# Kernel optimization log

Hardware: AMD Instinct MI355X
Metric: run time of the kernel (lower is better)

The kernel has to match this reference:

```python
import jax, jax.numpy as jnp
import numpy as np

# Model dims (match init_kwargs)
B, L, D = 1, 2048, 1024
DI = 2048          # D_inner
N = 16             # SSM state size
DR = 64            # delta_rank
K = 4              # conv_1d_size
EPS = 1e-5
DELTA_MIN, DELTA_MAX, DELTA_FLOOR = 1e-3, 1e-1, 1e-4


def setup_inputs() -> dict:
    key = jax.random.key(0)
    ks = jax.random.split(key, 9)
    g = lambda i, shape, scale: (jax.random.normal(ks[i], shape, jnp.float32) * scale)
    x = g(0, (B, L, D), 1.0)
    rms_w = jnp.ones((D,), jnp.float32)
    in_proj_w = g(1, (D, 2 * DI), D ** -0.5)           # Linear D -> 2*DI, no bias
    conv_w = g(2, (DI, K), 0.3)                         # depthwise conv kernel
    conv_b = g(3, (DI,), 0.1)
    bcd_w = g(4, (DI, 2 * N + DR), DI ** -0.5)          # to_BCdelta, no bias
    dup_w = g(5, (DR, DI), DR ** -0.5)                  # delta_upscale weight
    # delta_upscale bias: inverse-softplus of log-uniform samples in [delta_min, delta_max]
    u = jax.random.uniform(ks[6], (DI,), jnp.float32)
    samples = jnp.clip(jnp.exp(u * (np.log(DELTA_MAX) - np.log(DELTA_MIN)) + np.log(DELTA_MIN)), DELTA_FLOOR)
    dup_b = samples + jnp.log(-jnp.expm1(-samples))
    # log(-A) with A = -[1..N] repeated over channels (S4D-real init)
    log_minus_A = jnp.tile(jnp.log(jnp.arange(1, N + 1, dtype=jnp.float32))[None, :], (DI, 1))
    D_param = jnp.ones((DI,), jnp.float32)              # skip parameter D
    out_proj_w = g(7, (DI, D), DI ** -0.5)              # Linear DI -> D, no bias
    return {"x": x, "rms_w": rms_w, "in_proj_w": in_proj_w, "conv_w": conv_w,
            "conv_b": conv_b, "bcd_w": bcd_w, "dup_w": dup_w, "dup_b": dup_b,
            "log_minus_A": log_minus_A, "D_param": D_param, "out_proj_w": out_proj_w}


def reference(x, rms_w, in_proj_w, conv_w, conv_b, bcd_w, dup_w, dup_b,
              log_minus_A, D_param, out_proj_w):
    b, l, _ = x.shape
    # RMSNorm
    xn = x * jax.lax.rsqrt(jnp.mean(x * x, axis=-1, keepdims=True) + EPS) * rms_w
    # in_proj and split into ssm branch / gating residual branch
    proj = xn @ in_proj_w                                  # (b,l,2*DI)
    xs, res = proj[..., :DI], proj[..., DI:]
    # causal depthwise conv1d (torch pads K-1 both sides then truncates -> left-pad only)
    xp = jnp.pad(xs, ((0, 0), (K - 1, 0), (0, 0)))         # (b,l+K-1,DI)
    conv = sum(xp[:, k:k + l, :] * conv_w[:, k] for k in range(K)) + conv_b
    xc = jax.nn.silu(conv)                                 # (b,l,DI)
    # S6 block
    bcd = xc @ bcd_w                                       # (b,l,DR+2N)
    delta_lr = bcd[..., :DR]
    Bm = bcd[..., DR:DR + N]                               # (b,l,N)
    Cm = bcd[..., DR + N:]                                 # (b,l,N)
    delta = jax.nn.softplus(delta_lr @ dup_w + dup_b)      # (b,l,DI)
    A = -jnp.exp(log_minus_A)                              # (DI,N)
    A_bar = jnp.exp(jnp.einsum('bld,dn->bldn', delta, A))  # (b,l,DI,N)
    B_bar_x = jnp.einsum('bld,bln,bld->bldn', delta, Bm, xc)
    # sequential selective scan: h_t = A_bar_t * h_{t-1} + B_bar_x_t
    def step(h, ab_bx):
        ab, bx = ab_bx
        h = ab * h + bx
        return h, h
    h0 = jnp.zeros((b, DI, N), x.dtype)
    _, hs = jax.lax.scan(step, h0, (jnp.swapaxes(A_bar, 0, 1), jnp.swapaxes(B_bar_x, 0, 1)))
    # hs: (l,b,DI,N); project out with C and add skip D
    y = jnp.einsum('bln,lbdn->bld', Cm, hs) + xc * D_param
    # gate, out_proj, residual
    y = y * jax.nn.silu(res)
    return y @ out_proj_w + x
```

## Files before the change

### kernel.cpp

```cpp
#include <hip/hip_runtime.h>
#include <hip/hip_bf16.h>
#include <math.h>

#define Lseq 2048
#define Dmod 1024
#define DI   2048
#define Nst  16
#define DRr  64
#define NCHUNK 32
#define LCHUNK 64
#define SPLITK 16
#define OSPLIT 4

typedef unsigned short u16;
typedef float  f32x4  __attribute__((ext_vector_type(4)));
typedef short  short8 __attribute__((ext_vector_type(8)));

__device__ __forceinline__ float sigmoidf_(float x) { return 1.f / (1.f + expf(-x)); }
__device__ __forceinline__ float softplusf_(float x) {
    return fmaxf(x, 0.f) + log1pf(expf(-fabsf(x)));
}
__device__ __forceinline__ u16 f2bf(float x) {
    union { float f; unsigned u; } v; v.f = x;
    unsigned r = (v.u + 0x7fffu + ((v.u >> 16) & 1u)) >> 16;
    return (u16)r;
}
__device__ __forceinline__ float bf2f(u16 h) {
    union { unsigned u; float f; } v; v.u = ((unsigned)h) << 16; return v.f;
}
__device__ __forceinline__ void async16(const void* g, void* l) {
    __builtin_amdgcn_global_load_lds((__attribute__((address_space(1))) void*)g,
                                     (__attribute__((address_space(3))) void*)l, 16, 0, 0);
}

struct __align__(8) u16x4 { u16 x, y, z, w; };

__global__ __launch_bounds__(256) void rmsnorm_split_k(const float* __restrict__ x,
                                                       const float* __restrict__ w,
                                                       u16* __restrict__ xh,
                                                       u16* __restrict__ xl) {
    int row = blockIdx.x;
    int tid = threadIdx.x;
    float4 v = reinterpret_cast<const float4*>(x + (size_t)row * Dmod)[tid];
    float ss = v.x * v.x + v.y * v.y + v.z * v.z + v.w * v.w;
    #pragma unroll
    for (int m = 32; m >= 1; m >>= 1) ss += __shfl_xor(ss, m);
    __shared__ float s4[4];
    if ((tid & 63) == 0) s4[tid >> 6] = ss;
    __syncthreads();
    float tot = s4[0] + s4[1] + s4[2] + s4[3];
    float scale = rsqrtf(tot * (1.0f / Dmod) + 1e-5f);
    float4 wv = reinterpret_cast<const float4*>(w)[tid];
    float o[4] = {v.x * scale * wv.x, v.y * scale * wv.y,
                  v.z * scale * wv.z, v.w * scale * wv.w};
    u16x4 H, L;
    u16* hp = &H.x; u16* lp = &L.x;
    #pragma unroll
    for (int q = 0; q < 4; q++) {
        u16 h = f2bf(o[q]); hp[q] = h; lp[q] = f2bf(o[q] - bf2f(h));
    }
    reinterpret_cast<u16x4*>(xh + (size_t)row * Dmod)[tid] = H;
    reinterpret_cast<u16x4*>(xl + (size_t)row * Dmod)[tid] = L;
}

__device__ __forceinline__ void wsplit_body(const float* __restrict__ W, int R, int Cn,
                                            int bx, int by, float (*t)[33],
                                            u16* __restrict__ Th, u16* __restrict__ Tl) {
    int r0 = by * 32, c0 = bx * 32;
    int tr = threadIdx.x >> 3;
    int tc4 = (threadIdx.x & 7) * 4;
    float4 v = *reinterpret_cast<const float4*>(&W[(size_t)(r0 + tr) * Cn + c0 + tc4]);
    t[tr][tc4 + 0] = v.x; t[tr][tc4 + 1] = v.y;
    t[tr][tc4 + 2] = v.z; t[tr][tc4 + 3] = v.w;
    __syncthreads();
    u16x4 H, L;
    u16* hp = &H.x; u16* lp = &L.x;
    #pragma unroll
    for (int q = 0; q < 4; q++) {
        float xv = t[tc4 + q][tr];
        u16 h = f2bf(xv); hp[q] = h; lp[q] = f2bf(xv - bf2f(h));
    }
    size_t o = (size_t)(c0 + tr) * R + r0 + tc4;
    *reinterpret_cast<u16x4*>(&Th[o]) = H;
    *reinterpret_cast<u16x4*>(&Tl[o]) = L;
}

__global__ __launch_bounds__(256) void wsplitT_k(const float* __restrict__ W, int R, int Cn,
                                                 u16* __restrict__ Th, u16* __restrict__ Tl) {
    __shared__ float t[32][33];
    wsplit_body(W, R, Cn, blockIdx.x, blockIdx.y, t, Th, Tl);
}

__global__ __launch_bounds__(256) void wsplit3_k(const float* __restrict__ Wo,
                                                 const float* __restrict__ Wb,
                                                 const float* __restrict__ Wd,
                                                 u16* WoH, u16* WoL,
                                                 u16* bwTH, u16* bwTL,
                                                 u16* dwTH, u16* dwTL) {
    __shared__ float t[32][33];
    int b = blockIdx.x;
    if (b < 2048) {
        wsplit_body(Wo, 2048, 1024, b & 31, b >> 5, t, WoH, WoL);
    } else if (b < 2240) {
        int bb = b - 2048;
        wsplit_body(Wb, 2048, 96, bb % 3, bb / 3, t, bwTH, bwTL);
    } else {
        int bb = b - 2240;
        wsplit_body(Wd, 64, 2048, bb & 63, bb >> 6, t, dwTH, dwTL);
    }
}

template <int BM, int BN, int EPI>
__global__ __launch_bounds__(256) void gemm_mfma3(
    const u16* __restrict__ Ah, const u16* __restrict__ Al,
    const u16* __restrict__ Bh, const u16* __restrict__ Bl,
    float* __restrict__ C, float* __restrict__ C2, const float* __restrict__ aux,
    int M, int N, int K) {
    constexpr int BK = 32;
    constexpr int MF = BM / 32, NF = BN / 32;
    constexpr int CH_A = BM / 16, CH_B = BN / 16;
    __shared__ u16 AhT[BM][BK], AlT[BM][BK], BhT[BN][BK], BlT[BN][BK];
    const int tid = threadIdx.x, lane = tid & 63, wid = tid >> 6;
    const int wr = wid >> 1, wc = wid & 1;
    const int lr = lane & 15, lk = (lane >> 4) * 8;
    const int bm0 = blockIdx.y * BM, bn0 = blockIdx.x * BN;
    const int srow = lane >> 2, scol = (lane & 3) * 8;

    int kbeg = 0, kend = K;
    if (EPI == 5) {
        int ks = K / gridDim.z;
        kbeg = blockIdx.z * ks;
        kend = kbeg + ks;
    }

    f32x4 acc[MF][NF];
    #pragma unroll
    for (int i = 0; i < MF; i++)
        #pragma unroll
        for (int j = 0; j < NF; j++) acc[i][j] = (f32x4){0.f, 0.f, 0.f, 0.f};

    for (int k0 = kbeg; k0 < kend; k0 += BK) {
        int ci = 0;
        #pragma unroll
        for (int c = 0; c < CH_A; c++, ci++) if ((ci & 3) == wid) {
            size_t g = (size_t)(bm0 + c * 16 + srow) * K + (k0 + scol);
            async16(Ah + g, (u16*)&AhT[0][0] + c * 512 + lane * 8);
        }
        #pragma unroll
        for (int c = 0; c < CH_A; c++, ci++) if ((ci & 3) == wid) {
            size_t g = (size_t)(bm0 + c * 16 + srow) * K + (k0 + scol);
            async16(Al + g, (u16*)&AlT[0][0] + c * 512 + lane * 8);
        }
        #pragma unroll
        for (int c = 0; c < CH_B; c++, ci++) if ((ci & 3) == wid) {
            size_t g = (size_t)(bn0 + c * 16 + srow) * K + (k0 + scol);
            async16(Bh + g, (u16*)&BhT[0][0] + c * 512 + lane * 8);
        }
        #pragma unroll
        for (int c = 0; c < CH_B; c++, ci++) if ((ci & 3) == wid) {
            size_t g = (size_t)(bn0 + c * 16 + srow) * K + (k0 + scol);
            async16(Bl + g, (u16*)&BlT[0][0] + c * 512 + lane * 8);
        }
        __syncthreads();

        short8 ah[MF], al[MF], bh[NF], bl[NF];
        #pragma unroll
        for (int i = 0; i < MF; i++) {
            int r = wr * (MF * 16) + i * 16 + lr;
            ah[i] = *(const short8*)&AhT[r][lk];
            al[i] = *(const short8*)&AlT[r][lk];
        }
        #pragma unroll
        for (int j = 0; j < NF; j++) {
            int r = wc * (NF * 16) + j * 16 + lr;
            bh[j] = *(const short8*)&BhT[r][lk];
            bl[j] = *(const short8*)&BlT[r][lk];
        }
        #pragma unroll
        for (int i = 0; i < MF; i++)
            #pragma unroll
            for (int j = 0; j < NF; j++) {
                acc[i][j] = __builtin_amdgcn_mfma_f32_16x16x32_bf16(ah[i], bh[j], acc[i][j], 0, 0, 0);
                acc[i][j] = __builtin_amdgcn_mfma_f32_16x16x32_bf16(ah[i], bl[j], acc[i][j], 0, 0, 0);
                acc[i][j] = __builtin_amdgcn_mfma_f32_16x16x32_bf16(al[i], bh[j], acc[i][j], 0, 0, 0);
            }
        __syncthreads();
    }

    float* Cp = C;
    if (EPI == 5) Cp = C + (size_t)blockIdx.z * M * N;
    #pragma unroll
    for (int i = 0; i < MF; i++)
        #pragma unroll
        for (int j = 0; j < NF; j++) {
            int rowg = bm0 + wr * (MF * 16) + i * 16 + (lane >> 4) * 4;
            int colg = bn0 + wc * (NF * 16) + j * 16 + lr;
            #pragma unroll
            for (int q = 0; q < 4; q++) {
                float v = acc[i][j][q];
                if (EPI == 5) {
                    Cp[(size_t)(rowg + q) * N + colg] = v;
                } else if (EPI == 2) {
                    C[(size_t)(rowg + q) * N + colg] = softplusf_(v + aux[colg]);
                } else if (EPI == 4) {
                    if (colg < DI) C[(size_t)(rowg + q) * DI + colg] = v;
                    else C2[(size_t)(rowg + q) * DI + (colg - DI)] = v * sigmoidf_(v);
                }
            }
        }
}

__global__ __launch_bounds__(256) void bcd_reduce_k(const float* __restrict__ partial,
                                                    float* __restrict__ bcd,
                                                    u16* __restrict__ bH,
                                                    u16* __restrict__ bL) {
    const int NT = Lseq * 96;
    int t = blockIdx.x * 256 + threadIdx.x;
    float s = 0.f;
    #pragma unroll
    for (int z = 0; z < SPLITK; z++) s += partial[(size_t)z * NT + t];
    bcd[t] = s;
    int col = t % 96, row = t / 96;
    if (col < DRr) {
        u16 h = f2bf(s);
        bH[(size_t)row * DRr + col] = h;
        bL[(size_t)row * DRr + col] = f2bf(s - bf2f(h));
    }
}

__global__ __launch_bounds__(256) void out_reduce_k(const float* __restrict__ part,
                                                    const float* __restrict__ x,
                                                    float* __restrict__ out) {
    int t = blockIdx.x * 256 + threadIdx.x;
    const size_t NT = (size_t)Lseq * Dmod;
    float4 xv = reinterpret_cast<const float4*>(x)[t];
    float4 o = xv;
    #pragma unroll
    for (int z = 0; z < OSPLIT; z++) {
        float4 p = reinterpret_cast<const float4*>(part + (size_t)z * NT)[t];
        o.x += p.x; o.y += p.y; o.z += p.z; o.w += p.w;
    }
    reinterpret_cast<float4*>(out)[t] = o;
}

__global__ __launch_bounds__(256) void conv_silu_k(const float* __restrict__ xs,
                                                   const float* __restrict__ cw,
                                                   const float* __restrict__ cb,
                                                   u16* __restrict__ xcH,
                                                   u16* __restrict__ xcL) {
    int d = blockIdx.x * 256 + threadIdx.x;
    int l = blockIdx.y;
    float4 w = reinterpret_cast<const float4*>(cw)[d];
    float wk[4] = {w.x, w.y, w.z, w.w};
    float s = cb[d];
    #pragma unroll
    for (int k = 0; k < 4; k++) {
        int ls = l - 3 + k;
        if (ls >= 0) s = fmaf(xs[(size_t)ls * DI + d], wk[k], s);
    }
    float v = s * sigmoidf_(s);
    size_t o = (size_t)l * DI + d;
    u16 h = f2bf(v);
    xcH[o] = h;
    xcL[o] = f2bf(v - bf2f(h));
}

__global__ __launch_bounds__(256) void scan1_k(const float* __restrict__ delta,
                                               const u16* __restrict__ xcH,
                                               const u16* __restrict__ xcL,
                                               const float* __restrict__ bcd,
                                               const float* __restrict__ lmA,
                                               float* __restrict__ Pb,
                                               float* __restrict__ Sb) {
    __shared__ float Bs[LCHUNK][16];
    const int tid = threadIdx.x;
    const int d = (blockIdx.x * 256 + tid) >> 1;
    const int half = tid & 1;
    const int c = blockIdx.y;
    const int l0 = c * LCHUNK;
    {
        int row = tid >> 2, q = (tid & 3) * 4;
        float4 v = *reinterpret_cast<const float4*>(&bcd[(size_t)(l0 + row) * 96 + DRr + q]);
        *reinterpret_cast<float4*>(&Bs[row][q]) = v;
    }
    __syncthreads();
    float negA[8], h[8];
    #pragma unroll
    for (int j = 0; j < 8; j++) {
        negA[j] = -__expf(lmA[(size_t)d * Nst + half * 8 + j]);
        h[j] = 0.f;
    }
    float sdv = 0.f;
    for (int l = 0; l < LCHUNK; ++l) {
        size_t o = (size_t)(l0 + l) * DI + d;
        float dv = delta[o];
        float xcv = bf2f(xcH[o]) + bf2f(xcL[o]);
        sdv += dv;
        float dvx = dv * xcv;
        #pragma unroll
        for (int j = 0; j < 8; j++) {
            float a = __expf(dv * negA[j]);
            h[j] = fmaf(a, h[j], dvx * Bs[l][half * 8 + j]);
        }
    }
    size_t base = ((size_t)c * DI + d) * Nst + half * 8;
    #pragma unroll
    for (int j = 0; j < 8; j++) {
        Pb[base + j] = __expf(sdv * negA[j]);
        Sb[base + j] = h[j];
    }
}

__global__ __launch_bounds__(256) void scan2_k(float* __restrict__ PH,
                                               const float* __restrict__ Sb) {
    int t = blockIdx.x * 256 + threadIdx.x;
    float H = 0.f;
    for (int c = 0; c < NCHUNK; c++) {
        size_t idx = (size_t)c * (DI * Nst) + t;
        float P = PH[idx], S = Sb[idx];
        PH[idx] = H;
        H = S + P * H;
    }
}

__global__ __launch_bounds__(256) void scan3_k(const float* __restrict__ delta,
                                               const u16* __restrict__ xcH,
                                               const u16* __restrict__ xcL,
                                               const float* __restrict__ bcd,
                                               const float* __restrict__ lmA,
                                               const float* __restrict__ Dp,
                                               const float* __restrict__ gate,
                                               const float* __restrict__ Hinit,
                                               u16* __restrict__ yH,
                                               u16* __restrict__ yL) {
    __shared__ float BCs[LCHUNK][32];
    const int tid = threadIdx.x;
    const int d = (blockIdx.x * 256 + tid) >> 1;
    const int half = tid & 1;
    const int c = blockIdx.y;
    const int l0 = c * LCHUNK;
    #pragma unroll
    for (int i = 0; i < 2; i++) {
        int idx = tid + 256 * i;
        int row = idx >> 3, q = (idx & 7) * 4;
        float4 v = *reinterpret_cast<const float4*>(&bcd[(size_t)(l0 + row) * 96 + DRr + q]);
        *reinterpret_cast<float4*>(&BCs[row][q]) = v;
    }
    __syncthreads();
    float negA[8], h[8];
    size_t hbase = ((size_t)c * DI + d) * Nst + half * 8;
    #pragma unroll
    for (int j = 0; j < 8; j++) {
        negA[j] = -__expf(lmA[(size_t)d * Nst + half * 8 + j]);
        h[j] = Hinit[hbase + j];
    }
    float Dpv = Dp[d];
    for (int l = 0; l < LCHUNK; ++l) {
        size_t o = (size_t)(l0 + l) * DI + d;
        float dv = delta[o];
        float xcv = bf2f(xcH[o]) + bf2f(xcL[o]);
        float dvx = dv * xcv;
        float yp = 0.f;
        #pragma unroll
        for (int j = 0; j < 8; j++) {
            float a = __expf(dv * negA[j]);
            h[j] = fmaf(a, h[j], dvx * BCs[l][half * 8 + j]);
            yp = fmaf(BCs[l][16 + half * 8 + j], h[j], yp);
        }
        yp += __shfl_xor(yp, 1);
        if (half == 0) {
            float yv = (yp + xcv * Dpv) * gate[o];
            u16 hq = f2bf(yv);
            yH[o] = hq;
            yL[o] = f2bf(yv - bf2f(hq));
        }
    }
}

extern "C" void kernel_launch(void* const* d_in, const int* in_sizes, int n_in,
                              void* d_out, int out_size, void* d_ws, size_t ws_size,
                              hipStream_t stream) {
    const float* x          = (const float*)d_in[0];
    const float* rms_w      = (const float*)d_in[1];
    const float* in_proj_w  = (const float*)d_in[2];
    const float* conv_w     = (const float*)d_in[3];
    const float* conv_b     = (const float*)d_in[4];
    const float* bcd_w      = (const float*)d_in[5];
    const float* dup_w      = (const float*)d_in[6];
    const float* dup_b      = (const float*)d_in[7];
    const float* lmA        = (const float*)d_in[8];
    const float* Dp         = (const float*)d_in[9];
    const float* out_proj_w = (const float*)d_in[10];
    float* out = (float*)d_out;
    char*  W   = (char*)d_ws;

    const size_t MB = 1ull << 20;
    u16*   WiH  = (u16*)(W + 0);
    u16*   WiL  = (u16*)(W + 8 * MB);
    float* delta= (float*)(W + 0);
    float* xs   = (float*)(W + 16 * MB);
    float* part = (float*)(W + 16 * MB);
    u16*   bwTH = (u16*)(W + 28 * MB);
    u16*   bwTL = (u16*)(W + 28 * MB + 384 * 1024);
    u16*   dwTH = (u16*)(W + 28 * MB + 768 * 1024);
    u16*   dwTL = (u16*)(W + 28 * MB + 1024 * 1024);
    u16*   bcdH = (u16*)(W + 28 * MB + 1280 * 1024);
    u16*   bcdL = (u16*)(W + 28 * MB + 1536 * 1024);
    float* Sb   = (float*)(W + 16 * MB);
    u16*   yH   = (u16*)(W + 16 * MB);
    u16*   yL   = (u16*)(W + 24 * MB);
    float* gate = (float*)(W + 32 * MB);
    u16*   xcH  = (u16*)(W + 48 * MB);
    u16*   xcL  = (u16*)(W + 56 * MB);
    float* opart= (float*)(W + 32 * MB);
    u16*   xnH  = (u16*)(W + 64 * MB);
    u16*   xnL  = (u16*)(W + 68 * MB);
    u16*   WoH  = (u16*)(W + 64 * MB);
    u16*   WoL  = (u16*)(W + 68 * MB);
    float* bcd  = (float*)(W + 72 * MB);
    float* Pb   = (float*)(W + 73 * MB);

    rmsnorm_split_k<<<Lseq, 256, 0, stream>>>(x, rms_w, xnH, xnL);
    wsplitT_k<<<dim3(4096 / 32, 1024 / 32), 256, 0, stream>>>(in_proj_w, 1024, 4096, WiH, WiL);
    gemm_mfma3<128, 128, 4><<<dim3(4096 / 128, Lseq / 128), 256, 0, stream>>>(
        xnH, xnL, WiH, WiL, xs, gate, nullptr, Lseq, 2 * DI, Dmod);
    conv_silu_k<<<dim3(DI / 256, Lseq), 256, 0, stream>>>(xs, conv_w, conv_b, xcH, xcL);
    wsplit3_k<<<2368, 256, 0, stream>>>(out_proj_w, bcd_w, dup_w,
                                        WoH, WoL, bwTH, bwTL, dwTH, dwTL);
    gemm_mfma3<128, 96, 5><<<dim3(1, Lseq / 128, SPLITK), 256, 0, stream>>>(
        xcH, xcL, bwTH, bwTL, part, nullptr, nullptr, Lseq, 96, DI);
    bcd_reduce_k<<<Lseq * 96 / 256, 256, 0, stream>>>(part, bcd, bcdH, bcdL);
    gemm_mfma3<128, 128, 2><<<dim3(DI / 128, Lseq / 128), 256, 0, stream>>>(
        bcdH, bcdL, dwTH, dwTL, delta, nullptr, dup_b, Lseq, DI, DRr);
    scan1_k<<<dim3(16, NCHUNK), 256, 0, stream>>>(delta, xcH, xcL, bcd, lmA, Pb, Sb);
    scan2_k<<<dim3(DI * Nst / 256), 256, 0, stream>>>(Pb, Sb);
    scan3_k<<<dim3(16, NCHUNK), 256, 0, stream>>>(delta, xcH, xcL, bcd, lmA, Dp, gate, Pb, yH, yL);
    gemm_mfma3<128, 128, 5><<<dim3(Dmod / 128, Lseq / 128, OSPLIT), 256, 0, stream>>>(
        yH, yL, WoH, WoL, opart, nullptr, nullptr, Lseq, Dmod, DI);
    out_reduce_k<<<Lseq * Dmod / 1024, 256, 0, stream>>>(opart, x, out);
}
```

Measured before the change: 258.3 us.

## Double-buffer LDS tiles in split-bf16 MFMA GEMM and shrink delta GEMM tile

The shared GEMM kernel now keeps two LDS buffers per operand, so the next K-tile is fetched asynchronously while MFMAs run on the current one. This replaces the two full barriers per iteration with one wait-and-barrier. The aim is to hide global-load latency across every GEMM launch in the pipeline. The delta-upscale GEMM also moves to 64-row tiles, which doubles its block count for more parallelism on a K=64 problem. The cost is double the LDS per block, which can lower occupancy.

Measured after the change: 248.2 us. 3.9% less time.

```diff
diff --git a/kernel.cpp b/kernel.cpp
--- a/kernel.cpp
+++ b/kernel.cpp
@@ -119,7 +119,7 @@
     constexpr int BK = 32;
     constexpr int MF = BM / 32, NF = BN / 32;
     constexpr int CH_A = BM / 16, CH_B = BN / 16;
-    __shared__ u16 AhT[BM][BK], AlT[BM][BK], BhT[BN][BK], BlT[BN][BK];
+    __shared__ u16 AhT[2][BM][BK], AlT[2][BM][BK], BhT[2][BN][BK], BlT[2][BN][BK];
     const int tid = threadIdx.x, lane = tid & 63, wid = tid >> 6;
     const int wr = wid >> 1, wc = wid & 1;
     const int lr = lane & 15, lk = (lane >> 4) * 8;
@@ -132,50 +132,61 @@
         kbeg = blockIdx.z * ks;
         kend = kbeg + ks;
     }
-
-    f32x4 acc[MF][NF];
-    #pragma unroll
-    for (int i = 0; i < MF; i++)
-        #pragma unroll
-        for (int j = 0; j < NF; j++) acc[i][j] = (f32x4){0.f, 0.f, 0.f, 0.f};
-
-    for (int k0 = kbeg; k0 < kend; k0 += BK) {
+    const int nt = (kend - kbeg) / BK;
+
+    auto STAGE = [&](int buf, int k0) {
         int ci = 0;
         #pragma unroll
         for (int c = 0; c < CH_A; c++, ci++) if ((ci & 3) == wid) {
             size_t g = (size_t)(bm0 + c * 16 + srow) * K + (k0 + scol);
-            async16(Ah + g, (u16*)&AhT[0][0] + c * 512 + lane * 8);
+            async16(Ah + g, (u16*)&AhT[buf][0][0] + c * 512 + lane * 8);
         }
         #pragma unroll
         for (int c = 0; c < CH_A; c++, ci++) if ((ci & 3) == wid) {
             size_t g = (size_t)(bm0 + c * 16 + srow) * K + (k0 + scol);
-            async16(Al + g, (u16*)&AlT[0][0] + c * 512 + lane * 8);
+            async16(Al + g, (u16*)&AlT[buf][0][0] + c * 512 + lane * 8);
         }
         #pragma unroll
         for (int c = 0; c < CH_B; c++, ci++) if ((ci & 3) == wid) {
             size_t g = (size_t)(bn0 + c * 16 + srow) * K + (k0 + scol);
-            async16(Bh + g, (u16*)&BhT[0][0] + c * 512 + lane * 8);
+            async16(Bh + g, (u16*)&BhT[buf][0][0] + c * 512 + lane * 8);
         }
         #pragma unroll
         for (int c = 0; c < CH_B; c++, ci++) if ((ci & 3) == wid) {
             size_t g = (size_t)(bn0 + c * 16 + srow) * K + (k0 + scol);
-            async16(Bl + g, (u16*)&BlT[0][0] + c * 512 + lane * 8);
-        }
-        __syncthreads();
+            async16(Bl + g, (u16*)&BlT[buf][0][0] + c * 512 + lane * 8);
+        }
+    };
+
+    f32x4 acc[MF][NF];
+    #pragma unroll
+    for (int i = 0; i < MF; i++)
+        #pragma unroll
+        for (int j = 0; j < NF; j++) acc[i][j] = (f32x4){0.f, 0.f, 0.f, 0.f};
+
+    STAGE(0, kbeg);
+    asm volatile("s_waitcnt vmcnt(0)" ::: "memory");
+    __builtin_amdgcn_s_barrier();
+
+    for (int t = 0; t < nt; ++t) {
+        const int cur = t & 1;
+        if (t + 1 < nt) STAGE(cur ^ 1, kbeg + (t + 1) * BK);
 
         short8 ah[MF], al[MF], bh[NF], bl[NF];
         #pragma unroll
         for (int i = 0; i < MF; i++) {
             int r = wr * (MF * 16) + i * 16 + lr;
-            ah[i] = *(const short8*)&AhT[r][lk];
-            al[i] = *(const short8*)&AlT[r][lk];
+            ah[i] = *(const short8*)&AhT[cur][r][lk];
+            al[i] = *(const short8*)&AlT[cur][r][lk];
         }
         #pragma unroll
         for (int j = 0; j < NF; j++) {
             int r = wc * (NF * 16) + j * 16 + lr;
-            bh[j] = *(const short8*)&BhT[r][lk];
-            bl[j] = *(const short8*)&BlT[r][lk];
-        }
+            bh[j] = *(const short8*)&BhT[cur][r][lk];
+            bl[j] = *(const short8*)&BlT[cur][r][lk];
+        }
+        asm volatile("s_waitcnt lgkmcnt(0)" ::: "memory");
+        __builtin_amdgcn_sched_barrier(0);
         #pragma unroll
         for (int i = 0; i < MF; i++)
             #pragma unroll
@@ -184,7 +195,10 @@
                 acc[i][j] = __builtin_amdgcn_mfma_f32_16x16x32_bf16(ah[i], bl[j], acc[i][j], 0, 0, 0);
                 acc[i][j] = __builtin_amdgcn_mfma_f32_16x16x32_bf16(al[i], bh[j], acc[i][j], 0, 0, 0);
             }
-        __syncthreads();
+        if (t + 1 < nt) {
+            asm volatile("s_waitcnt vmcnt(0)" ::: "memory");
+            __builtin_amdgcn_s_barrier();
+        }
     }
 
     float* Cp = C;
@@ -430,7 +444,7 @@
     gemm_mfma3<128, 96, 5><<<dim3(1, Lseq / 128, SPLITK), 256, 0, stream>>>(
         xcH, xcL, bwTH, bwTL, part, nullptr, nullptr, Lseq, 96, DI);
     bcd_reduce_k<<<Lseq * 96 / 256, 256, 0, stream>>>(part, bcd, bcdH, bcdL);
-    gemm_mfma3<128, 128, 2><<<dim3(DI / 128, Lseq / 128), 256, 0, stream>>>(
+    gemm_mfma3<64, 128, 2><<<dim3(DI / 128, Lseq / 64), 256, 0, stream>>>(
         bcdH, bcdL, dwTH, dwTL, delta, nullptr, dup_b, Lseq, DI, DRr);
     scan1_k<<<dim3(16, NCHUNK), 256, 0, stream>>>(delta, xcH, xcL, bcd, lmA, Pb, Sb);
     scan2_k<<<dim3(DI * Nst / 256), 256, 0, stream>>>(Pb, Sb);
```
